# Kernel optimization log

Measured on AMD Instinct MI355X. Metric: run time of the kernel, lower is better.

Reference implementation:

```python
import jax, jax.numpy as jnp
import numpy as np

B, IN, OUT = 8192, 1024, 1024


def setup_inputs() -> dict:
    key = jax.random.key(0)
    k1, k2 = jax.random.split(key)
    x = jax.random.normal(k1, (B, IN), dtype=jnp.float32)
    W_seed = jax.random.normal(k2, (IN, OUT), dtype=jnp.float32) / np.sqrt(IN).astype(np.float32)
    b_seed = jnp.zeros((OUT,), dtype=jnp.float32)
    W_sig = jnp.zeros((2,), dtype=jnp.float32)  # mixture logits over ['dense','Toeplitz']
    b_sig = jnp.zeros((2,), dtype=jnp.float32)  # mixture logits over ['dense','None']
    A_sig = jnp.zeros((2,), dtype=jnp.float32)  # mixture logits over ['linear','relu']
    return {"x": x, "W_seed": W_seed, "b_seed": b_seed,
            "W_sig": W_sig, "b_sig": b_sig, "A_sig": A_sig}


def _toeplitz_from_seed(W_seed):
    # seed_vec = [W_seed[0, out-1], ..., W_seed[0, 1], W_seed[0,0], ..., W_seed[in-1,0]]
    in_sz, out_sz = W_seed.shape
    seed_vec = jnp.concatenate([W_seed[0, -1:0:-1], W_seed[:, 0]])  # [out-1 + in]
    # W_toep[i, j] = seed_vec[i - j + out - 1]
    idx = jnp.arange(in_sz)[:, None] - jnp.arange(out_sz)[None, :] + (out_sz - 1)
    return seed_vec[idx]  # [in, out]


def reference(x, W_seed, b_seed, W_sig, b_sig, A_sig):
    W_toep = _toeplitz_from_seed(W_seed)
    w_s = jax.nn.softmax(W_sig)
    W_core = w_s[0] * W_seed + w_s[1] * W_toep          # softmax-weighted weight mixture
    b_s = jax.nn.softmax(b_sig)
    b_core = b_s[0] * b_seed                             # 'None' branch contributes zeros
    out = x @ W_core + b_core                            # [B, out]
    a_s = jax.nn.softmax(A_sig)
    return a_s[0] * out + a_s[1] * jax.nn.relu(out)      # activation mixture
```

## Files before the change

### kernel.cpp

```cpp
#include <hip/hip_runtime.h>

typedef unsigned short ushort_t;
typedef __bf16 bf16x8 __attribute__((ext_vector_type(8)));
typedef float f32x4 __attribute__((ext_vector_type(4)));

#define AS1 __attribute__((address_space(1)))
#define AS3 __attribute__((address_space(3)))

__device__ __forceinline__ ushort_t f2bf(float f) {
    unsigned u = __builtin_bit_cast(unsigned, f);
    u = (u + 0x7fffu + ((u >> 16) & 1u)) >> 16;
    return (ushort_t)u;
}

__device__ __forceinline__ void async16(void* lds, const void* g) {
    __builtin_amdgcn_global_load_lds((const AS1 unsigned int*)g,
                                     (AS3 unsigned int*)lds, 16, 0, 0);
}

__device__ __forceinline__ void softmax2(const float* __restrict__ sig, float& s0, float& s1) {
    float a = sig[0], b = sig[1];
    float m = fmaxf(a, b);
    float e0 = __expf(a - m), e1 = __expf(b - m);
    float inv = 1.0f / (e0 + e1);
    s0 = e0 * inv; s1 = e1 * inv;
}

__device__ __forceinline__ float toep_val(const float* __restrict__ Wseed, int k, int o) {
    return (k >= o) ? Wseed[(size_t)(k - o) << 10] : Wseed[o - k];
}

__global__ __launch_bounds__(256) void prep_w_kernel(const float* __restrict__ Wseed,
                                                     const float* __restrict__ Wsig,
                                                     ushort_t* __restrict__ Wt) {
    __shared__ float T[64][65];
    int bb = blockIdx.x;
    int k0 = (bb >> 4) * 64;
    int o0 = (bb & 15) * 64;
    int t = threadIdx.x;
    #pragma unroll
    for (int i = 0; i < 4; ++i) {
        int lin = t + i * 256;
        int kr = lin >> 4;
        int c4 = lin & 15;
        float4 v = *(const float4*)&Wseed[(size_t)(k0 + kr) * 1024 + o0 + c4 * 4];
        T[kr][c4 * 4 + 0] = v.x;
        T[kr][c4 * 4 + 1] = v.y;
        T[kr][c4 * 4 + 2] = v.z;
        T[kr][c4 * 4 + 3] = v.w;
    }
    __syncthreads();
    float s0, s1; softmax2(Wsig, s0, s1);
    #pragma unroll
    for (int i = 0; i < 2; ++i) {
        int lin = t + i * 256;
        int oo = lin >> 3;
        int kq = (lin & 7) * 8;
        unsigned r[4];
        #pragma unroll
        for (int q = 0; q < 4; ++q) {
            float v0 = s0 * T[kq + 2 * q + 0][oo] + s1 * toep_val(Wseed, k0 + kq + 2 * q + 0, o0 + oo);
            float v1 = s0 * T[kq + 2 * q + 1][oo] + s1 * toep_val(Wseed, k0 + kq + 2 * q + 1, o0 + oo);
            r[q] = (unsigned)f2bf(v0) | ((unsigned)f2bf(v1) << 16);
        }
        *(uint4*)&Wt[(size_t)(o0 + oo) * 1024 + k0 + kq] = make_uint4(r[0], r[1], r[2], r[3]);
    }
}

#define BM 128
#define BN 128
#define BK 32
#define NKT 32

__global__ __launch_bounds__(512, 4) void gemm_kernel(const float* __restrict__ Xf,
                                                      const ushort_t* __restrict__ Wt,
                                                      const float* __restrict__ bseed,
                                                      const float* __restrict__ bsig,
                                                      const float* __restrict__ asig,
                                                      float* __restrict__ out) {
    __shared__ ushort_t lds[36864];
    ushort_t* p0 = lds;
    ushort_t* p1 = lds + 12288;
    ushort_t* p2 = lds + 24576;

    const int t = threadIdx.x;
    const int wv = t >> 6;
    const int lane = t & 63;

    const int orig = blockIdx.x;
    const int g = orig & 7;
    const int within = orig >> 3;
    const int rb = g * 8 + (within >> 3);
    const int cb = within & 7;
    const int brow = rb * BM;
    const int bcol = cb * BN;

    const int ra = t >> 3;
    const int ca = (t & 7) ^ (ra & 7);
    const float* gAsw = Xf + (size_t)(brow + ra) * 1024 + 4 * ca;

    const int rbb = t >> 2;
    const int cbk = (t & 3) ^ ((rbb >> 1) & 3);
    const ushort_t* gBsw = Wt + (size_t)(bcol + rbb) * 1024 + 8 * cbk;

    f32x4 acc[2][4];
    #pragma unroll
    for (int i = 0; i < 2; ++i)
        #pragma unroll
        for (int j = 0; j < 4; ++j) acc[i][j] = (f32x4){0.f, 0.f, 0.f, 0.f};

    const int wr = (wv >> 1) * 32;
    const int wcn = (wv & 1) * 64;
    const int fr = lane & 15;
    const int kg = (lane >> 4) * 8;
    const int c0 = (lane >> 4) * 2;

    float bs0, bs1, as0, as1;
    softmax2(bsig, bs0, bs1);
    softmax2(asig, as0, as1);
    float bias[4];
    #pragma unroll
    for (int ni = 0; ni < 4; ++ni)
        bias[ni] = bs0 * bseed[bcol + wcn + ni * 16 + fr];
    asm volatile("" :: "v"(bias[0]), "v"(bias[1]), "v"(bias[2]), "v"(bias[3]),
                       "v"(as0), "v"(as1));
    asm volatile("" ::: "memory");

#define STAGE(buf, ko)                                             \
    do {                                                           \
        async16((buf) + wv * 512,        gAsw + (ko));             \
        async16((buf) + 4096 + wv * 512, gAsw + 65536 + (ko));     \
        async16((buf) + 8192 + wv * 512, gBsw + (ko));             \
    } while (0)

#define COMPUTE(buf)                                                               \
    do {                                                                           \
        const float* Af_ = (const float*)(buf);                                    \
        bf16x8 af[2], bf[4];                                                       \
        _Pragma("unroll")                                                          \
        for (int mi = 0; mi < 2; ++mi) {                                           \
            int row_ = wr + mi * 16 + fr;                                          \
            f32x4 lo_ = *(const f32x4*)&Af_[row_ * 32 + (((c0)     ^ (row_ & 7)) << 2)]; \
            f32x4 hi_ = *(const f32x4*)&Af_[row_ * 32 + (((c0 + 1) ^ (row_ & 7)) << 2)]; \
            bf16x8 a_;                                                             \
            _Pragma("unroll")                                                      \
            for (int j_ = 0; j_ < 4; ++j_) {                                       \
                a_[j_]     = (__bf16)lo_[j_];                                      \
                a_[4 + j_] = (__bf16)hi_[j_];                                      \
            }                                                                      \
            af[mi] = a_;                                                           \
        }                                                                          \
        _Pragma("unroll")                                                          \
        for (int ni = 0; ni < 4; ++ni) {                                           \
            int rb_ = wcn + ni * 16 + fr;                                          \
            int ch_ = ((kg >> 3) ^ ((rb_ >> 1) & 3)) << 3;                         \
            bf[ni] = *(const bf16x8*)&(buf)[8192 + rb_ * 32 + ch_];                \
        }                                                                          \
        _Pragma("unroll")                                                          \
        for (int mi = 0; mi < 2; ++mi)                                             \
            _Pragma("unroll")                                                      \
            for (int ni = 0; ni < 4; ++ni)                                         \
                acc[mi][ni] = __builtin_amdgcn_mfma_f32_16x16x32_bf16(             \
                    af[mi], bf[ni], acc[mi][ni], 0, 0, 0);                         \
    } while (0)

    STAGE(p0, 0);
    STAGE(p1, BK);
    asm volatile("s_waitcnt vmcnt(3)" ::: "memory");
    __builtin_amdgcn_s_barrier();

    for (int T = 0; T < NKT; ++T) {
        if (T + 2 < NKT) STAGE(p2, (size_t)(T + 2) * BK);
        COMPUTE(p0);
        if (T < NKT - 2)       { asm volatile("s_waitcnt vmcnt(3)" ::: "memory");
                                 __builtin_amdgcn_s_barrier(); }
        else if (T == NKT - 2) { asm volatile("s_waitcnt vmcnt(0)" ::: "memory");
                                 __builtin_amdgcn_s_barrier(); }
        ushort_t* tmp_ = p0; p0 = p1; p1 = p2; p2 = tmp_;
    }

    #pragma unroll
    for (int ni = 0; ni < 4; ++ni) {
        int col = bcol + wcn + ni * 16 + fr;
        #pragma unroll
        for (int mi = 0; mi < 2; ++mi) {
            int row = brow + wr + mi * 16 + (lane >> 4) * 4;
            #pragma unroll
            for (int r = 0; r < 4; ++r) {
                float v = acc[mi][ni][r] + bias[ni];
                out[(size_t)(row + r) * 1024 + col] = as0 * v + as1 * fmaxf(v, 0.f);
            }
        }
    }
#undef STAGE
#undef COMPUTE
}

__global__ __launch_bounds__(256) void naive_kernel(const float* __restrict__ x,
                                                    const float* __restrict__ Wseed,
                                                    const float* __restrict__ bseed,
                                                    const float* __restrict__ Wsig,
                                                    const float* __restrict__ bsig,
                                                    const float* __restrict__ asig,
                                                    float* __restrict__ out) {
    int idx = blockIdx.x * 256 + threadIdx.x;
    int b = idx >> 10, o = idx & 1023;
    float ws0, ws1, bs0, bs1, as0, as1;
    softmax2(Wsig, ws0, ws1);
    softmax2(bsig, bs0, bs1);
    softmax2(asig, as0, as1);
    float s = 0.f;
    const float* xr = x + (size_t)b * 1024;
    for (int k = 0; k < 1024; ++k) {
        float wc = ws0 * Wseed[((size_t)k << 10) + o] + ws1 * toep_val(Wseed, k, o);
        s += xr[k] * wc;
    }
    float v = s + bs0 * bseed[o];
    out[idx] = as0 * v + as1 * fmaxf(v, 0.f);
}

extern "C" void kernel_launch(void* const* d_in, const int* in_sizes, int n_in,
                              void* d_out, int out_size, void* d_ws, size_t ws_size,
                              hipStream_t stream) {
    const float* x     = (const float*)d_in[0];
    const float* Wseed = (const float*)d_in[1];
    const float* bseed = (const float*)d_in[2];
    const float* Wsig  = (const float*)d_in[3];
    const float* bsig  = (const float*)d_in[4];
    const float* Asig  = (const float*)d_in[5];
    float* out = (float*)d_out;

    const size_t need = (2u << 20) + 1024;
    if (ws_size < need) {
        naive_kernel<<<dim3(8192 * 1024 / 256), dim3(256), 0, stream>>>(
            x, Wseed, bseed, Wsig, bsig, Asig, out);
        return;
    }

    ushort_t* Wt = (ushort_t*)d_ws;

    prep_w_kernel<<<dim3(256), dim3(256), 0, stream>>>(Wseed, Wsig, Wt);
    gemm_kernel<<<dim3(512), dim3(512), 0, stream>>>(x, Wt, bseed, bsig, Asig, out);
}
```

Baseline: 39.18 us.

## Load fp32 activations directly into registers, stage only weights through LDS

The A (fp32 activation) tile no longer goes through LDS. Each lane loads its MFMA fragment straight from global memory into registers and double-buffers those registers across K steps. Only the bf16 weight tile stays in a triple-buffered LDS ring. This shrinks LDS per block from 72KB to 24KB, which could raise occupancy and removes the LDS round-trip for A. The cost is that each A row is now read redundantly by the two waves sharing it, global loads are less coalesced (32-byte chunks per lane), and vmcnt accounting becomes more fragile.

```diff
diff --git a/kernel.cpp b/kernel.cpp
--- a/kernel.cpp
+++ b/kernel.cpp
@@ -78,10 +78,10 @@
                                                       const float* __restrict__ bsig,
                                                       const float* __restrict__ asig,
                                                       float* __restrict__ out) {
-    __shared__ ushort_t lds[36864];
-    ushort_t* p0 = lds;
-    ushort_t* p1 = lds + 12288;
-    ushort_t* p2 = lds + 24576;
+    __shared__ ushort_t lds[12288];
+    ushort_t* b0 = lds;
+    ushort_t* b1 = lds + 4096;
+    ushort_t* b2 = lds + 8192;
 
     const int t = threadIdx.x;
     const int wv = t >> 6;
@@ -95,25 +95,22 @@
     const int brow = rb * BM;
     const int bcol = cb * BN;
 
-    const int ra = t >> 3;
-    const int ca = (t & 7) ^ (ra & 7);
-    const float* gAsw = Xf + (size_t)(brow + ra) * 1024 + 4 * ca;
-
     const int rbb = t >> 2;
     const int cbk = (t & 3) ^ ((rbb >> 1) & 3);
     const ushort_t* gBsw = Wt + (size_t)(bcol + rbb) * 1024 + 8 * cbk;
-
-    f32x4 acc[2][4];
-    #pragma unroll
-    for (int i = 0; i < 2; ++i)
-        #pragma unroll
-        for (int j = 0; j < 4; ++j) acc[i][j] = (f32x4){0.f, 0.f, 0.f, 0.f};
 
     const int wr = (wv >> 1) * 32;
     const int wcn = (wv & 1) * 64;
     const int fr = lane & 15;
     const int kg = (lane >> 4) * 8;
-    const int c0 = (lane >> 4) * 2;
+
+    const float* gAw = Xf + (size_t)(brow + wr + fr) * 1024 + kg;
+
+    f32x4 acc[2][4];
+    #pragma unroll
+    for (int i = 0; i < 2; ++i)
+        #pragma unroll
+        for (int j = 0; j < 4; ++j) acc[i][j] = (f32x4){0.f, 0.f, 0.f, 0.f};
 
     float bs0, bs1, as0, as1;
     softmax2(bsig, bs0, bs1);
@@ -126,58 +123,70 @@
                        "v"(as0), "v"(as1));
     asm volatile("" ::: "memory");
 
-#define STAGE(buf, ko)                                             \
+    f32x4 aE0, aE1, aE2, aE3, aO0, aO1, aO2, aO3;
+
+#define LOADA(r0_, r1_, r2_, r3_, ko)                              \
     do {                                                           \
-        async16((buf) + wv * 512,        gAsw + (ko));             \
-        async16((buf) + 4096 + wv * 512, gAsw + 65536 + (ko));     \
-        async16((buf) + 8192 + wv * 512, gBsw + (ko));             \
+        r0_ = *(const f32x4*)(gAw + (ko));                         \
+        r1_ = *(const f32x4*)(gAw + (ko) + 4);                     \
+        r2_ = *(const f32x4*)(gAw + 16384 + (ko));                 \
+        r3_ = *(const f32x4*)(gAw + 16384 + (ko) + 4);             \
     } while (0)
 
-#define COMPUTE(buf)                                                               \
+#define STAGEB(buf, ko) async16((buf) + wv * 512, gBsw + (ko))
+
+#define COMPUTE(r0_, r1_, r2_, r3_, Bbuf)                                          \
     do {                                                                           \
-        const float* Af_ = (const float*)(buf);                                    \
-        bf16x8 af[2], bf[4];                                                       \
+        bf16x8 af0, af1, bf[4];                                                    \
         _Pragma("unroll")                                                          \
-        for (int mi = 0; mi < 2; ++mi) {                                           \
-            int row_ = wr + mi * 16 + fr;                                          \
-            f32x4 lo_ = *(const f32x4*)&Af_[row_ * 32 + (((c0)     ^ (row_ & 7)) << 2)]; \
-            f32x4 hi_ = *(const f32x4*)&Af_[row_ * 32 + (((c0 + 1) ^ (row_ & 7)) << 2)]; \
-            bf16x8 a_;                                                             \
-            _Pragma("unroll")                                                      \
-            for (int j_ = 0; j_ < 4; ++j_) {                                       \
-                a_[j_]     = (__bf16)lo_[j_];                                      \
-                a_[4 + j_] = (__bf16)hi_[j_];                                      \
-            }                                                                      \
-            af[mi] = a_;                                                           \
+        for (int j_ = 0; j_ < 4; ++j_) {                                           \
+            af0[j_]     = (__bf16)r0_[j_];                                         \
+            af0[4 + j_] = (__bf16)r1_[j_];                                         \
+            af1[j_]     = (__bf16)r2_[j_];                                         \
+            af1[4 + j_] = (__bf16)r3_[j_];                                         \
         }                                                                          \
         _Pragma("unroll")                                                          \
         for (int ni = 0; ni < 4; ++ni) {                                           \
             int rb_ = wcn + ni * 16 + fr;                                          \
             int ch_ = ((kg >> 3) ^ ((rb_ >> 1) & 3)) << 3;                         \
-            bf[ni] = *(const bf16x8*)&(buf)[8192 + rb_ * 32 + ch_];                \
+            bf[ni] = *(const bf16x8*)&(Bbuf)[rb_ * 32 + ch_];                      \
         }                                                                          \
         _Pragma("unroll")                                                          \
-        for (int mi = 0; mi < 2; ++mi)                                             \
-            _Pragma("unroll")                                                      \
-            for (int ni = 0; ni < 4; ++ni)                                         \
-                acc[mi][ni] = __builtin_amdgcn_mfma_f32_16x16x32_bf16(             \
-                    af[mi], bf[ni], acc[mi][ni], 0, 0, 0);                         \
+        for (int ni = 0; ni < 4; ++ni) {                                           \
+            acc[0][ni] = __builtin_amdgcn_mfma_f32_16x16x32_bf16(af0, bf[ni],      \
+                                                                 acc[0][ni], 0, 0, 0); \
+            acc[1][ni] = __builtin_amdgcn_mfma_f32_16x16x32_bf16(af1, bf[ni],      \
+                                                                 acc[1][ni], 0, 0, 0); \
+        }                                                                          \
     } while (0)
 
-    STAGE(p0, 0);
-    STAGE(p1, BK);
-    asm volatile("s_waitcnt vmcnt(3)" ::: "memory");
-    __builtin_amdgcn_s_barrier();
-
-    for (int T = 0; T < NKT; ++T) {
-        if (T + 2 < NKT) STAGE(p2, (size_t)(T + 2) * BK);
-        COMPUTE(p0);
-        if (T < NKT - 2)       { asm volatile("s_waitcnt vmcnt(3)" ::: "memory");
-                                 __builtin_amdgcn_s_barrier(); }
-        else if (T == NKT - 2) { asm volatile("s_waitcnt vmcnt(0)" ::: "memory");
-                                 __builtin_amdgcn_s_barrier(); }
-        ushort_t* tmp_ = p0; p0 = p1; p1 = p2; p2 = tmp_;
-    }
+#define WAIT5() asm volatile("s_waitcnt vmcnt(5)" ::: "memory")
+#define WAIT0() asm volatile("s_waitcnt vmcnt(0)" ::: "memory")
+#define BAR()   __builtin_amdgcn_s_barrier()
+
+    LOADA(aE0, aE1, aE2, aE3, 0);
+    STAGEB(b0, 0);
+    STAGEB(b1, 32);
+    asm volatile("s_waitcnt vmcnt(1)" ::: "memory");
+    BAR();
+
+    for (int i = 0; i < 15; ++i) {
+        const int T = 2 * i;
+        LOADA(aO0, aO1, aO2, aO3, (size_t)(T + 1) * 32);
+        WAIT5(); BAR();
+        STAGEB(b2, (size_t)(T + 2) * 32);
+        COMPUTE(aE0, aE1, aE2, aE3, b0);
+        LOADA(aE0, aE1, aE2, aE3, (size_t)(T + 2) * 32);
+        WAIT5(); BAR();
+        STAGEB(b0, (size_t)(T + 3) * 32);
+        COMPUTE(aO0, aO1, aO2, aO3, b1);
+        ushort_t* tmp_ = b0; b0 = b2; b2 = b1; b1 = tmp_;
+    }
+    LOADA(aO0, aO1, aO2, aO3, 31 * 32);
+    WAIT5(); BAR();
+    COMPUTE(aE0, aE1, aE2, aE3, b0);
+    WAIT0(); BAR();
+    COMPUTE(aO0, aO1, aO2, aO3, b1);
 
     #pragma unroll
     for (int ni = 0; ni < 4; ++ni) {
@@ -192,8 +201,12 @@
             }
         }
     }
-#undef STAGE
+#undef LOADA
+#undef STAGEB
 #undef COMPUTE
+#undef WAIT5
+#undef WAIT0
+#undef BAR
 }
 
 __global__ __launch_bounds__(256) void naive_kernel(const float* __restrict__ x,
```

New measurement: 79.03 us. 2.02x slower.
